# Optimization experiments

Hardware: AMD Instinct MI355X
Metric: run time of the kernel (lower is better)

## Reference

```python
import jax, jax.numpy as jnp
import numpy as np

K = 20
SLOPE = 0.2


def _edge_conv(x, params):
    """DynamicEdgeConv: kNN graph on x, edge MLP on [x_i, x_j - x_i], max-aggregate.

    x: [B, N, D] -> [B, N, D_out]
    """
    sq = jnp.sum(x * x, axis=-1)  # [B, N]
    # squared euclidean distances [B, N, N]
    d = sq[:, :, None] + sq[:, None, :] - 2.0 * jnp.einsum('bnd,bmd->bnm', x, x)
    _, idx = jax.lax.top_k(-d, K)  # [B, N, K] nearest (incl. self, dist 0)
    xj = jax.vmap(lambda xb, ib: xb[ib])(x, idx)  # [B, N, K, D]
    xi = x[:, :, None, :]
    h = jnp.concatenate([jnp.broadcast_to(xi, xj.shape), xj - xi], axis=-1)  # [B,N,K,2D]
    for W, b in params:
        h = jax.nn.leaky_relu(h @ W + b, SLOPE)
    return jnp.max(h, axis=2)  # max aggregation over neighbors


def setup_inputs() -> dict:
    key = jax.random.key(0)
    ks = jax.random.split(key, 10)
    B, N = 8, 4096
    H = 64
    def lin(k, fi, fo):
        return jax.random.normal(k, (fi, fo), jnp.float32) * (1.0 / np.sqrt(fi))
    inp = {
        'pos': jax.random.normal(ks[0], (B, N, 3), jnp.float32),
        'w11': lin(ks[1], 6, H),   'b11': jnp.zeros((H,), jnp.float32),
        'w12': lin(ks[2], H, H),   'b12': jnp.zeros((H,), jnp.float32),
        'w13': lin(ks[3], H, H),   'b13': jnp.zeros((H,), jnp.float32),
        'w21': lin(ks[4], 2 * H, H), 'b21': jnp.zeros((H,), jnp.float32),
        'w22': lin(ks[5], H, H),   'b22': jnp.zeros((H,), jnp.float32),
        'w23': lin(ks[6], H, H),   'b23': jnp.zeros((H,), jnp.float32),
        'w31': lin(ks[7], 2 * H, H), 'b31': jnp.zeros((H,), jnp.float32),
        'w32': lin(ks[8], H, H),   'b32': jnp.zeros((H,), jnp.float32),
        'w33': lin(ks[9], H, H),   'b33': jnp.zeros((H,), jnp.float32),
    }
    return inp


def reference(pos, w11, b11, w12, b12, w13, b13,
              w21, b21, w22, b22, w23, b23,
              w31, b31, w32, b32, w33, b33):
    x = _edge_conv(pos, [(w11, b11), (w12, b12), (w13, b13)])
    x = _edge_conv(x, [(w21, b21), (w22, b22), (w23, b23)])
    x = _edge_conv(x, [(w31, b31), (w32, b32), (w33, b33)])
    return x
```

## Files before the change

kernel.cpp:

```cpp
#include <hip/hip_runtime.h>
#include <stdint.h>

#define BATCH 8
#define NPTS 4096
#define KNN 20
#define TILE 64
#define NTILES (NPTS / TILE)
#define BTHR 256
#define CAP 4
#define CAPMAX 8
constexpr float SLOPE = 0.2f;

typedef unsigned long long u64;
#define INIT_KEY 0xFF7FFFFFFFFFFFFFULL

__device__ __forceinline__ u64 pack_key(float d, unsigned j) {
    unsigned ub = __float_as_uint(d);
    ub = (ub & 0x80000000u) ? ~ub : (ub | 0x80000000u);
    return ((u64)ub << 32) | j;
}
__device__ __forceinline__ float key_hi_to_d(unsigned hi) {
    unsigned u = (hi & 0x80000000u) ? (hi ^ 0x80000000u) : ~hi;
    return __uint_as_float(u);
}
__device__ __forceinline__ void insert_key(u64 (&lst)[KNN], u64 c) {
    #pragma unroll
    for (int k = 0; k < KNN; ++k) {
        const u64 lo = (lst[k] < c) ? lst[k] : c;
        const u64 hi = (lst[k] < c) ? c : lst[k];
        lst[k] = lo; c = hi;
    }
}
__device__ __forceinline__ void flush_buf(u64 (&lst)[KNN], const u64* __restrict__ buft,
                                          int& cnt, float& tmax) {
    for (int i = 0; i < CAPMAX; ++i) {
        if (!__any(i < cnt)) break;
        if (i < cnt) {
            const u64 key = buft[i * BTHR];
            if (key < lst[KNN - 1]) insert_key(lst, key);
        }
    }
    cnt = 0;
    float m = key_hi_to_d((unsigned)(lst[KNN - 1] >> 32));
    m = fminf(m, __shfl_xor(m, 1));
    m = fminf(m, __shfl_xor(m, 2));
    tmax = m;
}

template<int D>
__global__ __launch_bounds__(BTHR) void knn3_kernel(
    const float* __restrict__ X, const float* __restrict__ sq,
    int* __restrict__ knn_idx)
{
    __shared__ alignas(16) float smem[17280];
    float* xq   = smem;
    float* xj   = smem + 4352;
    float* dist = smem + 8704;
    float* sqq  = smem + 13056;
    float* sqj  = smem + 13120;
    u64*   buf  = (u64*)(smem + 13184);
    u64*   lists = (u64*)smem;

    const int t = threadIdx.x;
    const int b = blockIdx.y;
    const int qbase = blockIdx.x * 64;
    const float* Xb  = X  + (size_t)b * NPTS * D;
    const float* sqb = sq + (size_t)b * NPTS;

    const int qg = t >> 4, jg = t & 15;
    const int q  = t >> 2, s  = t & 3;

    float4 aq[(D == 3) ? 4 : 1];
    float sqq_r[4];
    if constexpr (D == 3) {
        #pragma unroll
        for (int rr = 0; rr < 4; ++rr) {
            const float* qp = Xb + (size_t)(qbase + 4 * qg + rr) * 3;
            aq[rr].x = qp[0]; aq[rr].y = qp[1]; aq[rr].z = qp[2]; aq[rr].w = 0.f;
            sqq_r[rr] = sqb[qbase + 4 * qg + rr];
        }
        if (t < 64) {
            const float* row = Xb + (size_t)t * 3;
            xj[0 * 68 + t] = row[0];
            xj[1 * 68 + t] = row[1];
            xj[2 * 68 + t] = row[2];
            sqj[t] = sqb[t];
        }
    } else {
        #pragma unroll
        for (int ci = t; ci < 1024; ci += BTHR) {
            const int r = ci >> 4, c4 = ci & 15;
            *(float4*)&xq[r * 68 + 4 * c4] =
                *(const float4*)&Xb[(size_t)(qbase + r) * 64 + 4 * c4];
        }
        #pragma unroll
        for (int ci = t; ci < 1024; ci += BTHR) {
            const int r = ci >> 4, c4 = ci & 15;
            const int c4s = (c4 + (r >> 2)) & 15;
            *(float4*)&xj[r * 68 + 4 * c4s] =
                *(const float4*)&Xb[(size_t)r * 64 + 4 * c4];
        }
        if (t < 64) { sqq[t] = sqb[qbase + t]; sqj[t] = sqb[t]; }
    }
    __syncthreads();
    if constexpr (D != 3) {
        #pragma unroll
        for (int rr = 0; rr < 4; ++rr) sqq_r[rr] = sqq[4 * qg + rr];
    }

    const float* aP0 = &xq[(4 * qg + 0) * 68];
    const float* aP1 = &xq[(4 * qg + 1) * 68];
    const float* aP2 = &xq[(4 * qg + 2) * 68];
    const float* aP3 = &xq[(4 * qg + 3) * 68];
    const float* bP0 = &xj[(4 * jg + 0) * 68];
    const float* bP1 = &xj[(4 * jg + 1) * 68];
    const float* bP2 = &xj[(4 * jg + 2) * 68];
    const float* bP3 = &xj[(4 * jg + 3) * 68];
    float* dW = &dist[4 * qg * 68 + 4 * jg];
    const float* drow = &dist[q * 68 + s * 16];
    const float* sjP = &sqj[4 * jg];
    u64* const buft = buf + t;
    u64* bufc = buft;

    u64 lst[KNN];
    #pragma unroll
    for (int k = 0; k < KNN; ++k) lst[k] = INIT_KEY;
    float tmax = 3.402823466e38f;
    int cnt = 0;

    for (int tile = 0; tile < NTILES; ++tile) {
        if constexpr (D == 3) {
            float sj[4];
            #pragma unroll
            for (int cc = 0; cc < 4; ++cc) sj[cc] = sjP[cc];
            float4 bx, by, bz;
            bx.x = xj[0 * 68 + 4 * jg + 0]; bx.y = xj[0 * 68 + 4 * jg + 1];
            bx.z = xj[0 * 68 + 4 * jg + 2]; bx.w = xj[0 * 68 + 4 * jg + 3];
            by.x = xj[1 * 68 + 4 * jg + 0]; by.y = xj[1 * 68 + 4 * jg + 1];
            by.z = xj[1 * 68 + 4 * jg + 2]; by.w = xj[1 * 68 + 4 * jg + 3];
            bz.x = xj[2 * 68 + 4 * jg + 0]; bz.y = xj[2 * 68 + 4 * jg + 1];
            bz.z = xj[2 * 68 + 4 * jg + 2]; bz.w = xj[2 * 68 + 4 * jg + 3];
            #pragma unroll
            for (int rr = 0; rr < 4; ++rr) {
                float4 dv;
                dv.x = sqq_r[rr] + sj[0] - 2.f * (aq[rr].x * bx.x + aq[rr].y * by.x + aq[rr].z * bz.x);
                dv.y = sqq_r[rr] + sj[1] - 2.f * (aq[rr].x * bx.y + aq[rr].y * by.y + aq[rr].z * bz.y);
                dv.z = sqq_r[rr] + sj[2] - 2.f * (aq[rr].x * bx.z + aq[rr].y * by.z + aq[rr].z * bz.z);
                dv.w = sqq_r[rr] + sj[3] - 2.f * (aq[rr].x * bx.w + aq[rr].y * by.w + aq[rr].z * bz.w);
                *(float4*)&dW[rr * 68] = dv;
            }
        } else {
            float acc[4][4];
            #pragma unroll
            for (int rr = 0; rr < 4; ++rr)
                #pragma unroll
                for (int cc = 0; cc < 4; ++cc) acc[rr][cc] = 0.f;
            #pragma unroll
            for (int k = 0; k < 16; ++k) {
                const int ko = 4 * k;
                const int kxo = 4 * ((k + jg) & 15);
                float4 a[4], bv[4];
                a[0] = *(const float4*)&aP0[ko];
                a[1] = *(const float4*)&aP1[ko];
                a[2] = *(const float4*)&aP2[ko];
                a[3] = *(const float4*)&aP3[ko];
                bv[0] = *(const float4*)&bP0[kxo];
                bv[1] = *(const float4*)&bP1[kxo];
                bv[2] = *(const float4*)&bP2[kxo];
                bv[3] = *(const float4*)&bP3[kxo];
                #pragma unroll
                for (int rr = 0; rr < 4; ++rr)
                    #pragma unroll
                    for (int cc = 0; cc < 4; ++cc) {
                        float v = acc[rr][cc];
                        v = fmaf(a[rr].x, bv[cc].x, v);
                        v = fmaf(a[rr].y, bv[cc].y, v);
                        v = fmaf(a[rr].z, bv[cc].z, v);
                        v = fmaf(a[rr].w, bv[cc].w, v);
                        acc[rr][cc] = v;
                    }
            }
            float sj[4];
            #pragma unroll
            for (int cc = 0; cc < 4; ++cc) sj[cc] = sjP[cc];
            #pragma unroll
            for (int rr = 0; rr < 4; ++rr) {
                float4 dv;
                dv.x = sqq_r[rr] + sj[0] - 2.f * acc[rr][0];
                dv.y = sqq_r[rr] + sj[1] - 2.f * acc[rr][1];
                dv.z = sqq_r[rr] + sj[2] - 2.f * acc[rr][2];
                dv.w = sqq_r[rr] + sj[3] - 2.f * acc[rr][3];
                *(float4*)&dW[rr * 68] = dv;
            }
        }
        __syncthreads();

        if (tile + 1 < NTILES) {
            const int cb = (tile + 1) * TILE;
            if constexpr (D == 3) {
                if (t < 64) {
                    const float* row = Xb + (size_t)(cb + t) * 3;
                    xj[0 * 68 + t] = row[0];
                    xj[1 * 68 + t] = row[1];
                    xj[2 * 68 + t] = row[2];
                    sqj[t] = sqb[cb + t];
                }
            } else {
                #pragma unroll
                for (int ci = t; ci < 1024; ci += BTHR) {
                    const int r = ci >> 4, c4 = ci & 15;
                    const int c4s = (c4 + (r >> 2)) & 15;
                    *(float4*)&xj[r * 68 + 4 * c4s] =
                        *(const float4*)&Xb[(size_t)(cb + r) * 64 + 4 * c4];
                }
                if (t < 64) sqj[t] = sqb[cb + t];
            }
        }

        {
            const unsigned cbase = tile * TILE + s * 16;
            #pragma unroll
            for (int g = 0; g < 4; ++g) {
                const float4 dv = *(const float4*)&drow[g * 4];
                if (dv.x <= tmax) { *bufc = pack_key(dv.x, cbase + g * 4 + 0); bufc += BTHR; ++cnt; }
                if (dv.y <= tmax) { *bufc = pack_key(dv.y, cbase + g * 4 + 1); bufc += BTHR; ++cnt; }
                if (dv.z <= tmax) { *bufc = pack_key(dv.z, cbase + g * 4 + 2); bufc += BTHR; ++cnt; }
                if (dv.w <= tmax) { *bufc = pack_key(dv.w, cbase + g * 4 + 3); bufc += BTHR; ++cnt; }
                if (__any(cnt >= CAP)) { flush_buf(lst, buft, cnt, tmax); bufc = buft; }
            }
        }
        __syncthreads();
    }
    if (__any(cnt > 0)) flush_buf(lst, buft, cnt, tmax);

    #pragma unroll
    for (int k = 0; k < KNN; ++k) lists[t * KNN + k] = lst[k];
    __syncthreads();

    if (t < 64) {
        const u64* L0 = lists + (size_t)(t * 4 + 0) * KNN;
        const u64* L1 = L0 + KNN;
        const u64* L2 = L1 + KNN;
        const u64* L3 = L2 + KNN;
        int p0 = 0, p1 = 0, p2 = 0, p3 = 0;
        int* outp = knn_idx + ((size_t)b * NPTS + qbase + t) * KNN;
        for (int k = 0; k < KNN; ++k) {
            const u64 h0 = L0[p0], h1 = L1[p1], h2 = L2[p2], h3 = L3[p3];
            const u64 m01 = (h0 < h1) ? h0 : h1;
            const u64 m23 = (h2 < h3) ? h2 : h3;
            const u64 m   = (m01 < m23) ? m01 : m23;
            outp[k] = (int)(unsigned)(m & 0xffffffffu);
            if (m == h0) ++p0; else if (m == h1) ++p1; else if (m == h2) ++p2; else ++p3;
        }
    }
}

template<int D>
__global__ __launch_bounds__(256) void uc_kernel(
    const float* __restrict__ X, const float* __restrict__ W1,
    const float* __restrict__ b1, float* __restrict__ u, float* __restrict__ cvec,
    float* __restrict__ sqv) {
    __shared__ float Xs[16 * D];
    const int n0 = blockIdx.x * 16;
    const int t = threadIdx.x;
    for (int i = t; i < 16 * D; i += 256)
        Xs[i] = X[(size_t)n0 * D + i];
    __syncthreads();

    if (t < 16) {
        float s = 0.f;
        #pragma unroll
        for (int d = 0; d < D; ++d) { const float v = Xs[t * D + d]; s += v * v; }
        sqv[n0 + t] = s;
    }

    const int o = t & 63;
    const int pg = t >> 6;
    float va[4] = {0.f, 0.f, 0.f, 0.f};
    float vb[4] = {0.f, 0.f, 0.f, 0.f};
    for (int d = 0; d < D; ++d) {
        const float wa = W1[d * 64 + o];
        const float wb = W1[(D + d) * 64 + o];
        #pragma unroll
        for (int pi = 0; pi < 4; ++pi) {
            const float x = Xs[(pg * 4 + pi) * D + d];
            va[pi] += x * wa;
            vb[pi] += x * wb;
        }
    }
    const float bo = b1[o];
    #pragma unroll
    for (int pi = 0; pi < 4; ++pi) {
        const size_t n = (size_t)n0 + pg * 4 + pi;
        u[n * 64 + o] = vb[pi];
        cvec[n * 64 + o] = va[pi] - vb[pi] + bo;
    }
}

__device__ __forceinline__ void gemm_acc(const float* __restrict__ Xs,
                                         const float* __restrict__ Ws,
                                         const float* __restrict__ bias,
                                         float (&acc)[5][4], const int t) {
    const int rg = t >> 4, og = t & 15;
    #pragma unroll
    for (int oc = 0; oc < 4; ++oc) {
        const float bb = bias[4 * og + oc];
        #pragma unroll
        for (int rr = 0; rr < 5; ++rr) acc[rr][oc] = bb;
    }
    #pragma unroll
    for (int k4 = 0; k4 < 16; ++k4) {
        float4 xv[5];
        #pragma unroll
        for (int rr = 0; rr < 5; ++rr)
            xv[rr] = *(const float4*)&Xs[(5 * rg + rr) * 68 + 4 * k4];
        float4 wv[4];
        #pragma unroll
        for (int kk = 0; kk < 4; ++kk)
            wv[kk] = *(const float4*)&Ws[(4 * k4 + kk) * 64 + 4 * og];
        #pragma unroll
        for (int rr = 0; rr < 5; ++rr) {
            acc[rr][0] += xv[rr].x * wv[0].x + xv[rr].y * wv[1].x + xv[rr].z * wv[2].x + xv[rr].w * wv[3].x;
            acc[rr][1] += xv[rr].x * wv[0].y + xv[rr].y * wv[1].y + xv[rr].z * wv[2].y + xv[rr].w * wv[3].y;
            acc[rr][2] += xv[rr].x * wv[0].z + xv[rr].y * wv[1].z + xv[rr].z * wv[2].z + xv[rr].w * wv[3].z;
            acc[rr][3] += xv[rr].x * wv[0].w + xv[rr].y * wv[1].w + xv[rr].z * wv[2].w + xv[rr].w * wv[3].w;
        }
    }
}

__global__ __launch_bounds__(256) void edge_kernel(
    const float* __restrict__ u, const float* __restrict__ cvec,
    const int* __restrict__ knn_idx,
    const float* __restrict__ W2, const float* __restrict__ b2,
    const float* __restrict__ W3, const float* __restrict__ b3,
    float* __restrict__ out) {
    __shared__ alignas(16) float h1s[80 * 68];
    __shared__ alignas(16) float Ws[64 * 64];
    __shared__ float cs[256];
    __shared__ float mxs[16 * 64];
    __shared__ int idxs[80];

    const int t = threadIdx.x;
    const int p0 = blockIdx.x * 4;
    const int b = p0 >> 12;

    cs[t] = cvec[(size_t)p0 * 64 + t];
    if (t < 80) idxs[t] = knn_idx[(size_t)p0 * KNN + t];
    for (int i = t; i < 4096; i += 256) Ws[i] = W2[i];
    __syncthreads();

    {
        const int wave = t >> 6, lane = t & 63;
        for (int e = wave; e < 80; e += 4) {
            const int j = idxs[e];
            const float val = u[((size_t)(b << 12) + j) * 64 + lane];
            const float pre = cs[(e / 20) * 64 + lane] + val;
            h1s[e * 68 + lane] = (pre > 0.f) ? pre : SLOPE * pre;
        }
    }
    __syncthreads();

    float acc[5][4];
    gemm_acc(h1s, Ws, b2, acc, t);
    __syncthreads();

    {
        const int rg = t >> 4, og = t & 15;
        #pragma unroll
        for (int rr = 0; rr < 5; ++rr)
            #pragma unroll
            for (int oc = 0; oc < 4; ++oc) {
                float v = acc[rr][oc];
                v = (v > 0.f) ? v : SLOPE * v;
                h1s[(5 * rg + rr) * 68 + 4 * og + oc] = v;
            }
        for (int i = t; i < 4096; i += 256) Ws[i] = W3[i];
    }
    __syncthreads();

    gemm_acc(h1s, Ws, b3, acc, t);
    {
        const int rg = t >> 4, og = t & 15;
        #pragma unroll
        for (int oc = 0; oc < 4; ++oc) {
            float m = -1e30f;
            #pragma unroll
            for (int rr = 0; rr < 5; ++rr) {
                float v = acc[rr][oc];
                v = (v > 0.f) ? v : SLOPE * v;
                m = fmaxf(m, v);
            }
            mxs[rg * 64 + 4 * og + oc] = m;
        }
    }
    __syncthreads();

    const int p = t >> 6, col = t & 63;
    const float m = fmaxf(fmaxf(mxs[(4 * p + 0) * 64 + col], mxs[(4 * p + 1) * 64 + col]),
                          fmaxf(mxs[(4 * p + 2) * 64 + col], mxs[(4 * p + 3) * 64 + col]));
    out[(size_t)(p0 + p) * 64 + col] = m;
}

extern "C" void kernel_launch(void* const* d_in, const int* in_sizes, int n_in,
                              void* d_out, int out_size, void* d_ws, size_t ws_size,
                              hipStream_t stream) {
    const float* pos = (const float*)d_in[0];
    const float* w11 = (const float*)d_in[1];  const float* b11 = (const float*)d_in[2];
    const float* w12 = (const float*)d_in[3];  const float* b12 = (const float*)d_in[4];
    const float* w13 = (const float*)d_in[5];  const float* b13 = (const float*)d_in[6];
    const float* w21 = (const float*)d_in[7];  const float* b21 = (const float*)d_in[8];
    const float* w22 = (const float*)d_in[9];  const float* b22 = (const float*)d_in[10];
    const float* w23 = (const float*)d_in[11]; const float* b23 = (const float*)d_in[12];
    const float* w31 = (const float*)d_in[13]; const float* b31 = (const float*)d_in[14];
    const float* w32 = (const float*)d_in[15]; const float* b32 = (const float*)d_in[16];
    const float* w33 = (const float*)d_in[17]; const float* b33 = (const float*)d_in[18];

    const int BN = BATCH * NPTS;
    float* ws = (float*)d_ws;
    float* sqb = ws;
    int*   idx = (int*)(sqb + BN);
    float* x1  = (float*)(idx + (size_t)BN * KNN);
    float* ubuf = x1 + (size_t)BN * 64;
    float* cbuf = ubuf + (size_t)BN * 64;
    float* x2  = cbuf + (size_t)BN * 64;

    const dim3 knn_grid(NPTS / 64, BATCH);

    uc_kernel<3><<<BN / 16, 256, 0, stream>>>(pos, w11, b11, ubuf, cbuf, sqb);
    knn3_kernel<3><<<knn_grid, BTHR, 0, stream>>>(pos, sqb, idx);
    edge_kernel<<<BN / 4, 256, 0, stream>>>(ubuf, cbuf, idx, w12, b12, w13, b13, x1);

    uc_kernel<64><<<BN / 16, 256, 0, stream>>>(x1, w21, b21, ubuf, cbuf, sqb);
    knn3_kernel<64><<<knn_grid, BTHR, 0, stream>>>(x1, sqb, idx);
    edge_kernel<<<BN / 4, 256, 0, stream>>>(ubuf, cbuf, idx, w22, b22, w23, b23, x2);

    uc_kernel<64><<<BN / 16, 256, 0, stream>>>(x2, w31, b31, ubuf, cbuf, sqb);
    knn3_kernel<64><<<knn_grid, BTHR, 0, stream>>>(x2, sqb, idx);
    edge_kernel<<<BN / 4, 256, 0, stream>>>(ubuf, cbuf, idx, w32, b32, w33, b33, (float*)d_out);
}
```

Baseline: 2.591 ms.

## Split 64-dim kNN candidate range across blocks and merge partial top-k lists

```diff
diff --git a/kernel.cpp b/kernel.cpp
--- a/kernel.cpp
+++ b/kernel.cpp
@@ -6,6 +6,9 @@
 #define KNN 20
 #define TILE 64
 #define NTILES (NPTS / TILE)
+#define NSPLIT2 2
+#define CSPLIT (NPTS / NSPLIT2)
+#define NTILES_S (CSPLIT / TILE)
 #define BTHR 256
 #define CAP 4
 #define CAPMAX 8
@@ -31,6 +34,20 @@
         lst[k] = lo; c = hi;
     }
 }
+__device__ __forceinline__ float dot64_chain(const float4* __restrict__ xq,
+                                             const float* __restrict__ row) {
+    float acc = 0.f;
+    #pragma unroll
+    for (int k = 0; k < 16; ++k) {
+        const float4 b = *(const float4*)&row[4 * k];
+        acc = fmaf(xq[k].x, b.x, acc);
+        acc = fmaf(xq[k].y, b.y, acc);
+        acc = fmaf(xq[k].z, b.z, acc);
+        acc = fmaf(xq[k].w, b.w, acc);
+    }
+    return acc;
+}
+
 __device__ __forceinline__ void flush_buf(u64 (&lst)[KNN], const u64* __restrict__ buft,
                                           int& cnt, float& tmax) {
     for (int i = 0; i < CAPMAX; ++i) {
@@ -47,66 +64,202 @@
     tmax = m;
 }
 
-template<int D>
+#define APPEND_KEY(key)                                   \
+    do {                                                  \
+        const u64 _k = (key);                             \
+        f0 = (cnt == 0) ? _k : f0;                        \
+        f1 = (cnt == 1) ? _k : f1;                        \
+        f2 = (cnt == 2) ? _k : f2;                        \
+        f3 = (cnt == 3) ? _k : f3;                        \
+        f4 = (cnt == 4) ? _k : f4;                        \
+        f5 = (cnt == 5) ? _k : f5;                        \
+        f6 = (cnt == 6) ? _k : f6;                        \
+        f7 = (cnt == 7) ? _k : f7;                        \
+        ++cnt;                                            \
+    } while (0)
+
+#define FLUSH_REGS()                                                    \
+    do {                                                                \
+        if (cnt > 0 && f0 < lst[KNN - 1]) insert_key(lst, f0);          \
+        if (cnt > 1 && f1 < lst[KNN - 1]) insert_key(lst, f1);          \
+        if (cnt > 2 && f2 < lst[KNN - 1]) insert_key(lst, f2);          \
+        if (cnt > 3 && f3 < lst[KNN - 1]) insert_key(lst, f3);          \
+        if (__any(cnt > 4)) {                                           \
+            if (cnt > 4 && f4 < lst[KNN - 1]) insert_key(lst, f4);      \
+            if (cnt > 5 && f5 < lst[KNN - 1]) insert_key(lst, f5);      \
+            if (cnt > 6 && f6 < lst[KNN - 1]) insert_key(lst, f6);      \
+            if (cnt > 7 && f7 < lst[KNN - 1]) insert_key(lst, f7);      \
+        }                                                               \
+        cnt = 0;                                                        \
+        float m_ = key_hi_to_d((unsigned)(lst[KNN - 1] >> 32));         \
+        m_ = fminf(m_, __shfl_xor(m_, 1));                              \
+        m_ = fminf(m_, __shfl_xor(m_, 2));                              \
+        tmax = m_;                                                      \
+    } while (0)
+
 __global__ __launch_bounds__(BTHR) void knn3_kernel(
     const float* __restrict__ X, const float* __restrict__ sq,
     int* __restrict__ knn_idx)
 {
     __shared__ alignas(16) float smem[17280];
+    float* xj   = smem + 4352;
+    float* dist = smem + 8704;
+    float* sqj  = smem + 13120;
+    u64*   buf  = (u64*)(smem + 13184);
+    u64*   lists = (u64*)smem;
+
+    const int t = threadIdx.x;
+    const int b = blockIdx.y;
+    const int qbase = blockIdx.x * 64;
+    const float* Xb  = X  + (size_t)b * NPTS * 3;
+    const float* sqb = sq + (size_t)b * NPTS;
+
+    const int qg = t >> 4, jg = t & 15;
+    const int q  = t >> 2, s  = t & 3;
+
+    float4 aq[4];
+    float sqq_r[4];
+    #pragma unroll
+    for (int rr = 0; rr < 4; ++rr) {
+        const float* qp = Xb + (size_t)(qbase + 4 * qg + rr) * 3;
+        aq[rr].x = qp[0]; aq[rr].y = qp[1]; aq[rr].z = qp[2]; aq[rr].w = 0.f;
+        sqq_r[rr] = sqb[qbase + 4 * qg + rr];
+    }
+    if (t < 64) {
+        const float* row = Xb + (size_t)t * 3;
+        xj[0 * 68 + t] = row[0];
+        xj[1 * 68 + t] = row[1];
+        xj[2 * 68 + t] = row[2];
+        sqj[t] = sqb[t];
+    }
+    __syncthreads();
+
+    float* dW = &dist[4 * qg * 68 + 4 * jg];
+    const float* drow = &dist[q * 68 + s * 16];
+    const float* sjP = &sqj[4 * jg];
+    u64* const buft = buf + t;
+    u64* bufc = buft;
+
+    u64 lst[KNN];
+    #pragma unroll
+    for (int k = 0; k < KNN; ++k) lst[k] = INIT_KEY;
+    float tmax = 3.402823466e38f;
+    int cnt = 0;
+
+    for (int tile = 0; tile < NTILES; ++tile) {
+        {
+            float sj[4];
+            #pragma unroll
+            for (int cc = 0; cc < 4; ++cc) sj[cc] = sjP[cc];
+            float4 bx, by, bz;
+            bx.x = xj[0 * 68 + 4 * jg + 0]; bx.y = xj[0 * 68 + 4 * jg + 1];
+            bx.z = xj[0 * 68 + 4 * jg + 2]; bx.w = xj[0 * 68 + 4 * jg + 3];
+            by.x = xj[1 * 68 + 4 * jg + 0]; by.y = xj[1 * 68 + 4 * jg + 1];
+            by.z = xj[1 * 68 + 4 * jg + 2]; by.w = xj[1 * 68 + 4 * jg + 3];
+            bz.x = xj[2 * 68 + 4 * jg + 0]; bz.y = xj[2 * 68 + 4 * jg + 1];
+            bz.z = xj[2 * 68 + 4 * jg + 2]; bz.w = xj[2 * 68 + 4 * jg + 3];
+            #pragma unroll
+            for (int rr = 0; rr < 4; ++rr) {
+                float4 dv;
+                dv.x = sqq_r[rr] + sj[0] - 2.f * (aq[rr].x * bx.x + aq[rr].y * by.x + aq[rr].z * bz.x);
+                dv.y = sqq_r[rr] + sj[1] - 2.f * (aq[rr].x * bx.y + aq[rr].y * by.y + aq[rr].z * bz.y);
+                dv.z = sqq_r[rr] + sj[2] - 2.f * (aq[rr].x * bx.z + aq[rr].y * by.z + aq[rr].z * bz.z);
+                dv.w = sqq_r[rr] + sj[3] - 2.f * (aq[rr].x * bx.w + aq[rr].y * by.w + aq[rr].z * bz.w);
+                *(float4*)&dW[rr * 68] = dv;
+            }
+        }
+        __syncthreads();
+
+        if (tile + 1 < NTILES) {
+            const int cb = (tile + 1) * TILE;
+            if (t < 64) {
+                const float* row = Xb + (size_t)(cb + t) * 3;
+                xj[0 * 68 + t] = row[0];
+                xj[1 * 68 + t] = row[1];
+                xj[2 * 68 + t] = row[2];
+                sqj[t] = sqb[cb + t];
+            }
+        }
+
+        {
+            const unsigned cbase = tile * TILE + s * 16;
+            #pragma unroll
+            for (int g = 0; g < 4; ++g) {
+                const float4 dv = *(const float4*)&drow[g * 4];
+                if (dv.x <= tmax) { *bufc = pack_key(dv.x, cbase + g * 4 + 0); bufc += BTHR; ++cnt; }
+                if (dv.y <= tmax) { *bufc = pack_key(dv.y, cbase + g * 4 + 1); bufc += BTHR; ++cnt; }
+                if (dv.z <= tmax) { *bufc = pack_key(dv.z, cbase + g * 4 + 2); bufc += BTHR; ++cnt; }
+                if (dv.w <= tmax) { *bufc = pack_key(dv.w, cbase + g * 4 + 3); bufc += BTHR; ++cnt; }
+                if (__any(cnt >= CAP)) { flush_buf(lst, buft, cnt, tmax); bufc = buft; }
+            }
+        }
+        __syncthreads();
+    }
+    if (__any(cnt > 0)) flush_buf(lst, buft, cnt, tmax);
+
+    #pragma unroll
+    for (int k = 0; k < KNN; ++k) lists[t * KNN + k] = lst[k];
+    __syncthreads();
+
+    if (t < 64) {
+        const u64* L0 = lists + (size_t)(t * 4 + 0) * KNN;
+        const u64* L1 = L0 + KNN;
+        const u64* L2 = L1 + KNN;
+        const u64* L3 = L2 + KNN;
+        int p0 = 0, p1 = 0, p2 = 0, p3 = 0;
+        int* outp = knn_idx + ((size_t)b * NPTS + qbase + t) * KNN;
+        for (int k = 0; k < KNN; ++k) {
+            const u64 h0 = L0[p0], h1 = L1[p1], h2 = L2[p2], h3 = L3[p3];
+            const u64 m01 = (h0 < h1) ? h0 : h1;
+            const u64 m23 = (h2 < h3) ? h2 : h3;
+            const u64 m   = (m01 < m23) ? m01 : m23;
+            outp[k] = (int)(unsigned)(m & 0xffffffffu);
+            if (m == h0) ++p0; else if (m == h1) ++p1; else if (m == h2) ++p2; else ++p3;
+        }
+    }
+}
+
+__global__ __launch_bounds__(BTHR) void knn64s_kernel(
+    const float* __restrict__ X, const float* __restrict__ sq,
+    unsigned* __restrict__ part)
+{
+    __shared__ alignas(16) float smem[13184];
     float* xq   = smem;
     float* xj   = smem + 4352;
     float* dist = smem + 8704;
     float* sqq  = smem + 13056;
     float* sqj  = smem + 13120;
-    u64*   buf  = (u64*)(smem + 13184);
     u64*   lists = (u64*)smem;
 
     const int t = threadIdx.x;
-    const int b = blockIdx.y;
+    const int split = blockIdx.y, b = blockIdx.z;
     const int qbase = blockIdx.x * 64;
-    const float* Xb  = X  + (size_t)b * NPTS * D;
+    const int cstart = split * CSPLIT;
+    const float* Xb  = X  + (size_t)b * NPTS * 64;
     const float* sqb = sq + (size_t)b * NPTS;
+    const size_t BN = (size_t)BATCH * NPTS;
 
     const int qg = t >> 4, jg = t & 15;
     const int q  = t >> 2, s  = t & 3;
 
-    float4 aq[(D == 3) ? 4 : 1];
+    #pragma unroll
+    for (int ci = t; ci < 1024; ci += BTHR) {
+        const int r = ci >> 4, c4 = ci & 15;
+        *(float4*)&xq[r * 68 + 4 * c4] =
+            *(const float4*)&Xb[(size_t)(qbase + r) * 64 + 4 * c4];
+    }
+    #pragma unroll
+    for (int ci = t; ci < 1024; ci += BTHR) {
+        const int r = ci >> 4, c4 = ci & 15;
+        const int c4s = (c4 + (r >> 2)) & 15;
+        *(float4*)&xj[r * 68 + 4 * c4s] =
+            *(const float4*)&Xb[(size_t)(cstart + r) * 64 + 4 * c4];
+    }
+    if (t < 64) { sqq[t] = sqb[qbase + t]; sqj[t] = sqb[cstart + t]; }
+    __syncthreads();
     float sqq_r[4];
-    if constexpr (D == 3) {
-        #pragma unroll
-        for (int rr = 0; rr < 4; ++rr) {
-            const float* qp = Xb + (size_t)(qbase + 4 * qg + rr) * 3;
-            aq[rr].x = qp[0]; aq[rr].y = qp[1]; aq[rr].z = qp[2]; aq[rr].w = 0.f;
-            sqq_r[rr] = sqb[qbase + 4 * qg + rr];
-        }
-        if (t < 64) {
-            const float* row = Xb + (size_t)t * 3;
-            xj[0 * 68 + t] = row[0];
-            xj[1 * 68 + t] = row[1];
-            xj[2 * 68 + t] = row[2];
-            sqj[t] = sqb[t];
-        }
-    } else {
-        #pragma unroll
-        for (int ci = t; ci < 1024; ci += BTHR) {
-            const int r = ci >> 4, c4 = ci & 15;
-            *(float4*)&xq[r * 68 + 4 * c4] =
-                *(const float4*)&Xb[(size_t)(qbase + r) * 64 + 4 * c4];
-        }
-        #pragma unroll
-        for (int ci = t; ci < 1024; ci += BTHR) {
-            const int r = ci >> 4, c4 = ci & 15;
-            const int c4s = (c4 + (r >> 2)) & 15;
-            *(float4*)&xj[r * 68 + 4 * c4s] =
-                *(const float4*)&Xb[(size_t)r * 64 + 4 * c4];
-        }
-        if (t < 64) { sqq[t] = sqb[qbase + t]; sqj[t] = sqb[t]; }
-    }
-    __syncthreads();
-    if constexpr (D != 3) {
-        #pragma unroll
-        for (int rr = 0; rr < 4; ++rr) sqq_r[rr] = sqq[4 * qg + rr];
-    }
+    #pragma unroll
+    for (int rr = 0; rr < 4; ++rr) sqq_r[rr] = sqq[4 * qg + rr];
 
     const float* aP0 = &xq[(4 * qg + 0) * 68];
     const float* aP1 = &xq[(4 * qg + 1) * 68];
@@ -119,37 +272,16 @@
     float* dW = &dist[4 * qg * 68 + 4 * jg];
     const float* drow = &dist[q * 68 + s * 16];
     const float* sjP = &sqj[4 * jg];
-    u64* const buft = buf + t;
-    u64* bufc = buft;
 
     u64 lst[KNN];
     #pragma unroll
     for (int k = 0; k < KNN; ++k) lst[k] = INIT_KEY;
     float tmax = 3.402823466e38f;
     int cnt = 0;
-
-    for (int tile = 0; tile < NTILES; ++tile) {
-        if constexpr (D == 3) {
-            float sj[4];
-            #pragma unroll
-            for (int cc = 0; cc < 4; ++cc) sj[cc] = sjP[cc];
-            float4 bx, by, bz;
-            bx.x = xj[0 * 68 + 4 * jg + 0]; bx.y = xj[0 * 68 + 4 * jg + 1];
-            bx.z = xj[0 * 68 + 4 * jg + 2]; bx.w = xj[0 * 68 + 4 * jg + 3];
-            by.x = xj[1 * 68 + 4 * jg + 0]; by.y = xj[1 * 68 + 4 * jg + 1];
-            by.z = xj[1 * 68 + 4 * jg + 2]; by.w = xj[1 * 68 + 4 * jg + 3];
-            bz.x = xj[2 * 68 + 4 * jg + 0]; bz.y = xj[2 * 68 + 4 * jg + 1];
-            bz.z = xj[2 * 68 + 4 * jg + 2]; bz.w = xj[2 * 68 + 4 * jg + 3];
-            #pragma unroll
-            for (int rr = 0; rr < 4; ++rr) {
-                float4 dv;
-                dv.x = sqq_r[rr] + sj[0] - 2.f * (aq[rr].x * bx.x + aq[rr].y * by.x + aq[rr].z * bz.x);
-                dv.y = sqq_r[rr] + sj[1] - 2.f * (aq[rr].x * bx.y + aq[rr].y * by.y + aq[rr].z * bz.y);
-                dv.z = sqq_r[rr] + sj[2] - 2.f * (aq[rr].x * bx.z + aq[rr].y * by.z + aq[rr].z * bz.z);
-                dv.w = sqq_r[rr] + sj[3] - 2.f * (aq[rr].x * bx.w + aq[rr].y * by.w + aq[rr].z * bz.w);
-                *(float4*)&dW[rr * 68] = dv;
-            }
-        } else {
+    u64 f0 = 0, f1 = 0, f2 = 0, f3 = 0, f4 = 0, f5 = 0, f6 = 0, f7 = 0;
+
+    for (int tile = 0; tile < NTILES_S; ++tile) {
+        {
             float acc[4][4];
             #pragma unroll
             for (int rr = 0; rr < 4; ++rr)
@@ -195,43 +327,33 @@
         }
         __syncthreads();
 
-        if (tile + 1 < NTILES) {
-            const int cb = (tile + 1) * TILE;
-            if constexpr (D == 3) {
-                if (t < 64) {
-                    const float* row = Xb + (size_t)(cb + t) * 3;
-                    xj[0 * 68 + t] = row[0];
-                    xj[1 * 68 + t] = row[1];
-                    xj[2 * 68 + t] = row[2];
-                    sqj[t] = sqb[cb + t];
-                }
-            } else {
-                #pragma unroll
-                for (int ci = t; ci < 1024; ci += BTHR) {
-                    const int r = ci >> 4, c4 = ci & 15;
-                    const int c4s = (c4 + (r >> 2)) & 15;
-                    *(float4*)&xj[r * 68 + 4 * c4s] =
-                        *(const float4*)&Xb[(size_t)(cb + r) * 64 + 4 * c4];
-                }
-                if (t < 64) sqj[t] = sqb[cb + t];
-            }
+        if (tile + 1 < NTILES_S) {
+            const int cb = cstart + (tile + 1) * TILE;
+            #pragma unroll
+            for (int ci = t; ci < 1024; ci += BTHR) {
+                const int r = ci >> 4, c4 = ci & 15;
+                const int c4s = (c4 + (r >> 2)) & 15;
+                *(float4*)&xj[r * 68 + 4 * c4s] =
+                    *(const float4*)&Xb[(size_t)(cb + r) * 64 + 4 * c4];
+            }
+            if (t < 64) sqj[t] = sqb[cstart + (tile + 1) * TILE + t];
         }
 
         {
-            const unsigned cbase = tile * TILE + s * 16;
+            const unsigned cbase = cstart + tile * TILE + s * 16;
             #pragma unroll
             for (int g = 0; g < 4; ++g) {
                 const float4 dv = *(const float4*)&drow[g * 4];
-                if (dv.x <= tmax) { *bufc = pack_key(dv.x, cbase + g * 4 + 0); bufc += BTHR; ++cnt; }
-                if (dv.y <= tmax) { *bufc = pack_key(dv.y, cbase + g * 4 + 1); bufc += BTHR; ++cnt; }
-                if (dv.z <= tmax) { *bufc = pack_key(dv.z, cbase + g * 4 + 2); bufc += BTHR; ++cnt; }
-                if (dv.w <= tmax) { *bufc = pack_key(dv.w, cbase + g * 4 + 3); bufc += BTHR; ++cnt; }
-                if (__any(cnt >= CAP)) { flush_buf(lst, buft, cnt, tmax); bufc = buft; }
+                if (dv.x <= tmax) APPEND_KEY(pack_key(dv.x, cbase + g * 4 + 0));
+                if (dv.y <= tmax) APPEND_KEY(pack_key(dv.y, cbase + g * 4 + 1));
+                if (dv.z <= tmax) APPEND_KEY(pack_key(dv.z, cbase + g * 4 + 2));
+                if (dv.w <= tmax) APPEND_KEY(pack_key(dv.w, cbase + g * 4 + 3));
+                if (__any(cnt >= CAP)) FLUSH_REGS();
             }
         }
         __syncthreads();
     }
-    if (__any(cnt > 0)) flush_buf(lst, buft, cnt, tmax);
+    if (__any(cnt > 0)) FLUSH_REGS();
 
     #pragma unroll
     for (int k = 0; k < KNN; ++k) lists[t * KNN + k] = lst[k];
@@ -243,16 +365,52 @@
         const u64* L2 = L1 + KNN;
         const u64* L3 = L2 + KNN;
         int p0 = 0, p1 = 0, p2 = 0, p3 = 0;
-        int* outp = knn_idx + ((size_t)b * NPTS + qbase + t) * KNN;
+        #pragma unroll
         for (int k = 0; k < KNN; ++k) {
             const u64 h0 = L0[p0], h1 = L1[p1], h2 = L2[p2], h3 = L3[p3];
             const u64 m01 = (h0 < h1) ? h0 : h1;
             const u64 m23 = (h2 < h3) ? h2 : h3;
             const u64 m   = (m01 < m23) ? m01 : m23;
-            outp[k] = (int)(unsigned)(m & 0xffffffffu);
+            part[((size_t)split * KNN + k) * BN + (size_t)b * NPTS + qbase + t] =
+                (unsigned)(m & 0xffffffffu);
             if (m == h0) ++p0; else if (m == h1) ++p1; else if (m == h2) ++p2; else ++p3;
         }
     }
+}
+
+__global__ __launch_bounds__(256) void merge64_kernel(
+    const float* __restrict__ X, const float* __restrict__ sq,
+    const unsigned* __restrict__ part, int* __restrict__ idx) {
+    const int bq = blockIdx.x * 256 + threadIdx.x;
+    const int b = bq >> 12;
+    const int qn = bq & (NPTS - 1);
+    const float* Xb  = X  + (size_t)b * NPTS * 64;
+    const float* sqb = sq + (size_t)b * NPTS;
+    const size_t BN = (size_t)BATCH * NPTS;
+
+    float4 xq[16];
+    #pragma unroll
+    for (int k = 0; k < 16; ++k)
+        xq[k] = *(const float4*)&Xb[(size_t)qn * 64 + 4 * k];
+    const float sqq = sqb[qn];
+
+    u64 lst[KNN];
+    #pragma unroll
+    for (int k = 0; k < KNN; ++k) lst[k] = INIT_KEY;
+
+    #pragma unroll
+    for (int s = 0; s < NSPLIT2; ++s) {
+        for (int k = 0; k < KNN; ++k) {
+            const unsigned j = part[((size_t)s * KNN + k) * BN + bq];
+            const float dd = sqq + sqb[j] - 2.f * dot64_chain(xq, &Xb[(size_t)j * 64]);
+            const u64 key = pack_key(dd, j);
+            if (key < lst[KNN - 1]) insert_key(lst, key);
+        }
+    }
+    int* outp = idx + (size_t)bq * KNN;
+    #pragma unroll
+    for (int k = 0; k < KNN; ++k)
+        outp[k] = (int)(unsigned)(lst[k] & 0xffffffffu);
 }
 
 template<int D>
@@ -423,18 +581,23 @@
     float* ubuf = x1 + (size_t)BN * 64;
     float* cbuf = ubuf + (size_t)BN * 64;
     float* x2  = cbuf + (size_t)BN * 64;
-
-    const dim3 knn_grid(NPTS / 64, BATCH);
+    unsigned* part2 = (unsigned*)x2;
+    unsigned* part3 = (unsigned*)x1;
+
+    const dim3 knn3_grid(NPTS / 64, BATCH);
+    const dim3 knn64_grid(NPTS / 64, NSPLIT2, BATCH);
 
     uc_kernel<3><<<BN / 16, 256, 0, stream>>>(pos, w11, b11, ubuf, cbuf, sqb);
-    knn3_kernel<3><<<knn_grid, BTHR, 0, stream>>>(pos, sqb, idx);
+    knn3_kernel<<<knn3_grid, BTHR, 0, stream>>>(pos, sqb, idx);
     edge_kernel<<<BN / 4, 256, 0, stream>>>(ubuf, cbuf, idx, w12, b12, w13, b13, x1);
 
     uc_kernel<64><<<BN / 16, 256, 0, stream>>>(x1, w21, b21, ubuf, cbuf, sqb);
-    knn3_kernel<64><<<knn_grid, BTHR, 0, stream>>>(x1, sqb, idx);
+    knn64s_kernel<<<knn64_grid, BTHR, 0, stream>>>(x1, sqb, part2);
+    merge64_kernel<<<BN / 256, 256, 0, stream>>>(x1, sqb, part2, idx);
     edge_kernel<<<BN / 4, 256, 0, stream>>>(ubuf, cbuf, idx, w22, b22, w23, b23, x2);
 
     uc_kernel<64><<<BN / 16, 256, 0, stream>>>(x2, w31, b31, ubuf, cbuf, sqb);
-    knn3_kernel<64><<<knn_grid, BTHR, 0, stream>>>(x2, sqb, idx);
+    knn64s_kernel<<<knn64_grid, BTHR, 0, stream>>>(x2, sqb, part3);
+    merge64_kernel<<<BN / 256, 256, 0, stream>>>(x2, sqb, part3, idx);
     edge_kernel<<<BN / 4, 256, 0, stream>>>(ubuf, cbuf, idx, w32, b32, w33, b33, (float*)d_out);
 }
```

New measurement: 3.083 ms. 19.0% more time.
